# Optimization experiments

Measured on AMD Instinct MI355X. Metric: run time of the kernel, lower is better.

## Reference

```python
import jax, jax.numpy as jnp
import numpy as np

V, E, H, K, B, T = 50000, 128, 256, 9, 128, 512
HD = H // 2  # hidden per direction


def setup_inputs() -> dict:
    key = jax.random.key(0)
    ks = jax.random.split(key, 16)
    s = 0.1
    inp = {
        "x": jax.random.randint(ks[0], (B, T), 0, V),
        "emb": jax.random.normal(ks[1], (V, E), jnp.float32) * 0.02,
        "w_ih_f": jax.random.normal(ks[2], (4 * HD, E), jnp.float32) * s,
        "w_hh_f": jax.random.normal(ks[3], (4 * HD, HD), jnp.float32) * s,
        "b_ih_f": jax.random.normal(ks[4], (4 * HD,), jnp.float32) * s,
        "b_hh_f": jax.random.normal(ks[5], (4 * HD,), jnp.float32) * s,
        "w_ih_b": jax.random.normal(ks[6], (4 * HD, E), jnp.float32) * s,
        "w_hh_b": jax.random.normal(ks[7], (4 * HD, HD), jnp.float32) * s,
        "b_ih_b": jax.random.normal(ks[8], (4 * HD,), jnp.float32) * s,
        "b_hh_b": jax.random.normal(ks[9], (4 * HD,), jnp.float32) * s,
        "W_tag": jax.random.normal(ks[10], (K, H), jnp.float32) * s,
        "b_tag": jax.random.normal(ks[11], (K,), jnp.float32) * s,
        "start_trans": jax.random.normal(ks[12], (K,), jnp.float32) * s,
        "end_trans": jax.random.normal(ks[13], (K,), jnp.float32) * s,
        "trans": jax.random.normal(ks[14], (K, K), jnp.float32) * s,
    }
    return inp


def _lstm_dir(xs, w_ih, w_hh, b_ih, b_hh, reverse):
    # xs: [T, B, E]; PyTorch gate order: i, f, g, o
    Bsz = xs.shape[1]
    hd = w_hh.shape[1]
    b = b_ih + b_hh

    def step(carry, x_t):
        h, c = carry
        gates = x_t @ w_ih.T + h @ w_hh.T + b  # [B, 4*hd]
        i, f, g, o = jnp.split(gates, 4, axis=-1)
        i = jax.nn.sigmoid(i)
        f = jax.nn.sigmoid(f)
        g = jnp.tanh(g)
        o = jax.nn.sigmoid(o)
        c = f * c + i * g
        h = o * jnp.tanh(c)
        return (h, c), h

    init = (jnp.zeros((Bsz, hd), xs.dtype), jnp.zeros((Bsz, hd), xs.dtype))
    _, hs = jax.lax.scan(step, init, xs, reverse=reverse)
    return hs  # [T, B, hd], time-ordered


def _viterbi(emissions, start_trans, end_trans, trans):
    # emissions: [T, B, K]; returns best tag path [B, T] (torchcrf decode, no mask)
    score0 = start_trans[None, :] + emissions[0]  # [B, K]

    def step(score, emis_t):
        # score[b, i] + trans[i, j] -> best over i
        cand = score[:, :, None] + trans[None, :, :]  # [B, K, K]
        bp = jnp.argmax(cand, axis=1)                 # [B, K] best prev tag
        best = jnp.max(cand, axis=1)
        return best + emis_t, bp

    final_score, bps = jax.lax.scan(step, score0, emissions[1:])  # bps: [T-1, B, K]
    final_score = final_score + end_trans[None, :]
    last_tag = jnp.argmax(final_score, axis=-1)  # [B]

    def back(tag, bp):
        prev = jnp.take_along_axis(bp, tag[:, None], axis=1)[:, 0]
        return prev, prev

    _, path = jax.lax.scan(back, last_tag, bps, reverse=True)  # [T-1, B]
    tags = jnp.concatenate([path, last_tag[None, :]], axis=0)  # [T, B]
    return tags.T.astype(jnp.int32)  # [B, T]


def reference(x, emb, w_ih_f, w_hh_f, b_ih_f, b_hh_f,
              w_ih_b, w_hh_b, b_ih_b, b_hh_b,
              W_tag, b_tag, start_trans, end_trans, trans):
    xt = x.T                        # [T, B]
    e = emb[xt]                     # [T, B, E] embedding gather
    h_f = _lstm_dir(e, w_ih_f, w_hh_f, b_ih_f, b_hh_f, reverse=False)
    h_b = _lstm_dir(e, w_ih_b, w_hh_b, b_ih_b, b_hh_b, reverse=True)
    h = jnp.concatenate([h_f, h_b], axis=-1)  # [T, B, H]
    # dropout is identity at inference
    emissions = h @ W_tag.T + b_tag           # [T, B, K]
    return _viterbi(emissions, start_trans, end_trans, trans)
```

## Files before the change

kernel.cpp:

```cpp
#include <hip/hip_runtime.h>
#include <math.h>

#define TT 512
#define BB 128
#define KK 9

__device__ __forceinline__ float fast_sigmoid(float x) {
    const float LOG2E = 1.4426950408889634f;
    float e = __builtin_amdgcn_exp2f(-x * LOG2E);
    return __builtin_amdgcn_rcpf(1.0f + e);
}
__device__ __forceinline__ float fast_tanh(float x) {
    const float LOG2E = 1.4426950408889634f;
    float a = fabsf(x);
    float e = __builtin_amdgcn_exp2f(-2.0f * a * LOG2E);
    float t = (1.0f - e) * __builtin_amdgcn_rcpf(1.0f + e);
    return copysignf(t, x);
}

__global__ __launch_bounds__(256) void gather_e(
    const int* __restrict__ x, const float* __restrict__ emb,
    float* __restrict__ e)
{
    const int row  = blockIdx.x * 8 + (threadIdx.x >> 5);
    const int lane = threadIdx.x & 31;
    const int t = row >> 7;
    const int b = row & 127;
    const int tok = x[b * TT + t];
    const float4 v = *(const float4*)(emb + (size_t)tok * 128 + lane * 4);
    *(float4*)(e + (size_t)row * 128 + lane * 4) = v;
}

__global__ __launch_bounds__(256, 1) void input_gemm(
    const float* __restrict__ e,
    const float* __restrict__ w_ih_f, const float* __restrict__ w_ih_b,
    const float* __restrict__ b_ih_f, const float* __restrict__ b_hh_f,
    const float* __restrict__ b_ih_b, const float* __restrict__ b_hh_b,
    float* __restrict__ buf_f, float* __restrict__ buf_b,
    int t0f, int t0b)
{
    const int dir = blockIdx.z;
    const int s   = blockIdx.x;
    const int n0  = blockIdx.y * 128;
    const int t   = (dir ? t0b : t0f) + s;
    const float* w  = dir ? w_ih_b : w_ih_f;
    const float* bi = dir ? b_ih_b : b_ih_f;
    const float* bh = dir ? b_hh_b : b_hh_f;
    float* dst = dir ? buf_b : buf_f;

    __shared__ __align__(16) float As[128][132];
    __shared__ __align__(16) float Bs[128][4][36];

    const int tid = threadIdx.x;
    const int tx = tid & 15;
    const int ty = tid >> 4;
    const int li = tid & 127;
    const int kb = (tid >> 7) * 4;

    const float* arow = e + ((size_t)t * 128 + li) * 128;
    const float* wrow = w + (size_t)(n0 + li) * 128;

    float4 aR[16], bR[16];
    #pragma unroll
    for (int r = 0; r < 16; r++) aR[r] = *(const float4*)(arow + r * 8 + kb);
    #pragma unroll
    for (int r = 0; r < 16; r++) bR[r] = *(const float4*)(wrow + r * 8 + kb);

    const int bsub = li >> 5, boff = li & 31;
    #pragma unroll
    for (int r = 0; r < 16; r++) {
        As[r * 8 + kb + 0][li] = aR[r].x;
        As[r * 8 + kb + 1][li] = aR[r].y;
        As[r * 8 + kb + 2][li] = aR[r].z;
        As[r * 8 + kb + 3][li] = aR[r].w;
        Bs[r * 8 + kb + 0][bsub][boff] = bR[r].x;
        Bs[r * 8 + kb + 1][bsub][boff] = bR[r].y;
        Bs[r * 8 + kb + 2][bsub][boff] = bR[r].z;
        Bs[r * 8 + kb + 3][bsub][boff] = bR[r].w;
    }
    __syncthreads();

    float acc[8][8];
    #pragma unroll
    for (int i = 0; i < 8; i++)
        #pragma unroll
        for (int j = 0; j < 8; j++) acc[i][j] = 0.0f;

    #pragma unroll 8
    for (int k = 0; k < 128; k++) {
        float4 af0 = *(const float4*)&As[k][ty * 8];
        float4 af1 = *(const float4*)&As[k][ty * 8 + 4];
        float4 bf0 = *(const float4*)&Bs[k][tx >> 2][(tx & 3) * 8];
        float4 bf1 = *(const float4*)&Bs[k][tx >> 2][(tx & 3) * 8 + 4];
        float a_[8] = {af0.x, af0.y, af0.z, af0.w, af1.x, af1.y, af1.z, af1.w};
        float b_[8] = {bf0.x, bf0.y, bf0.z, bf0.w, bf1.x, bf1.y, bf1.z, bf1.w};
        #pragma unroll
        for (int i = 0; i < 8; i++)
            #pragma unroll
            for (int j = 0; j < 8; j++)
                acc[i][j] += a_[i] * b_[j];
    }

    const int nbase = n0 + tx * 8;
    float bias[8];
    #pragma unroll
    for (int j = 0; j < 8; j++) {
        int n = nbase + j;
        bias[j] = bi[n] + bh[n];
    }
    #pragma unroll
    for (int i = 0; i < 8; i++) {
        int brow = ty * 8 + i;
        float* o = dst + ((size_t)s * 128 + brow) * 512 + nbase;
        float4 v0, v1;
        v0.x = acc[i][0] + bias[0]; v0.y = acc[i][1] + bias[1];
        v0.z = acc[i][2] + bias[2]; v0.w = acc[i][3] + bias[3];
        v1.x = acc[i][4] + bias[4]; v1.y = acc[i][5] + bias[5];
        v1.z = acc[i][6] + bias[6]; v1.w = acc[i][7] + bias[7];
        *(float4*)o = v0;
        *(float4*)(o + 4) = v1;
    }
}

__global__ __launch_bounds__(512, 2) void lstm_chunk(
    const float* __restrict__ buf_f, const float* __restrict__ buf_b,
    const float* __restrict__ w_hh_f, const float* __restrict__ w_hh_b,
    float* __restrict__ h_all,
    float* __restrict__ h_state, float* __restrict__ c_state,
    int t0f, int t0b, int C, int init)
{
    const int dir = blockIdx.x >> 7;
    const int b   = blockIdx.x & 127;
    const int j   = threadIdx.x;
    const int w_  = j >> 6;
    const int l   = j & 63;
    const int m   = l >> 2;
    const int q   = l & 3;
    const int k   = w_ * 16 + m;
    const int r   = q * 128 + k;

    const float* whh = dir ? w_hh_b : w_hh_f;
    float wR[128];
    #pragma unroll
    for (int qq = 0; qq < 32; qq++) {
        float4 v = *(const float4*)(whh + (size_t)r * 128 + qq * 4);
        wR[4*qq+0] = v.x; wR[4*qq+1] = v.y; wR[4*qq+2] = v.z; wR[4*qq+3] = v.w;
    }

    __shared__ __align__(16) float h_lds[2][128];
    float c;
    if (init) {
        c = 0.0f;
        if (q == 0) h_lds[0][k] = 0.0f;
    } else {
        c = c_state[((size_t)dir * 128 + b) * 128 + k];
        if (q == 0) h_lds[0][k] = h_state[((size_t)dir * 128 + b) * 128 + k];
    }
    __syncthreads();

    const float* buf = dir ? buf_b : buf_f;
    const int t0     = dir ? t0b : t0f;
    const int  tl0   = dir ? (C - 1) : 0;
    const long lstep = dir ? -(long)(128 * 512) : (long)(128 * 512);

    const float* xp = buf + ((size_t)tl0 * 128 + b) * 512 + r;
    float xw = *xp;
    float h_reg = 0.0f;
    int   t_prev = 0;
    bool  have_store = false;

    for (int s = 0; s < C; s++) {
        const int t = t0 + (dir ? (C - 1 - s) : s);
        const int p = s & 1;
        const float* hprev = h_lds[p];

        float a0 = 0.f, a1 = 0.f, a2 = 0.f, a3 = 0.f;
        #pragma unroll
        for (int qq = 0; qq < 32; qq++) {
            float4 h4 = *(const float4*)&hprev[4 * qq];
            a0 += wR[4*qq+0] * h4.x;
            a1 += wR[4*qq+1] * h4.y;
            a2 += wR[4*qq+2] * h4.z;
            a3 += wR[4*qq+3] * h4.w;
        }
        float pre = xw + ((a0 + a1) + (a2 + a3));

        float act = (q == 2) ? fast_tanh(pre) : fast_sigmoid(pre);

        float f_ = __shfl_xor(act, 1);
        float g_ = __shfl_xor(act, 2);
        float o_ = __shfl_xor(act, 3);

        c = f_ * c + act * g_;
        h_reg = o_ * fast_tanh(c);
        if (q == 0) h_lds[p ^ 1][k] = h_reg;

        __syncthreads();

        if (s + 1 < C) { xp += lstep; xw = *xp; }
        if (q == 0)
            h_all[((size_t)t * BB + b) * 256 + dir * 128 + k] = h_reg;
        t_prev = t; have_store = true;
        (void)t_prev; (void)have_store;
    }

    if (q == 0) {
        h_state[((size_t)dir * 128 + b) * 128 + k] = h_reg;
        c_state[((size_t)dir * 128 + b) * 128 + k] = c;
    }
}

__global__ __launch_bounds__(256) void emis_kernel(
    const float* __restrict__ h_all, const float* __restrict__ W_tag,
    const float* __restrict__ b_tag, float* __restrict__ em_sum)
{
    const int wid  = threadIdx.x >> 6;
    const int lane = threadIdx.x & 63;
    const size_t m = (size_t)blockIdx.x * 4 + wid;
    const float4 hv = *(const float4*)(h_all + m * 256 + lane * 4);
    #pragma unroll
    for (int kk = 0; kk < KK; kk++) {
        const float4 wv = *(const float4*)(W_tag + kk * 256 + lane * 4);
        float p = hv.x * wv.x + hv.y * wv.y + hv.z * wv.z + hv.w * wv.w;
        #pragma unroll
        for (int off = 32; off > 0; off >>= 1) p += __shfl_down(p, off);
        if (lane == 0) em_sum[m * KK + kk] = p + b_tag[kk];
    }
}

__global__ __launch_bounds__(64) void viterbi_kernel(
    const float* __restrict__ em_sum,
    const float* __restrict__ start_trans, const float* __restrict__ end_trans,
    const float* __restrict__ trans, int* __restrict__ out)
{
    const int b = blockIdx.x;
    const int lane = threadIdx.x;
    __shared__ float em_s[TT * KK];
    __shared__ unsigned char bp[TT][KK];

    for (int f = lane; f < TT * KK; f += 64) {
        int t = f / KK, kk = f - t * KK;
        em_s[f] = em_sum[((size_t)t * BB + b) * KK + kk];
    }
    __syncthreads();

    float trans_col[KK];
    float score = -1e30f;
    if (lane < KK) {
        #pragma unroll
        for (int i = 0; i < KK; i++) trans_col[i] = trans[i * KK + lane];
        score = start_trans[lane] + em_s[lane];
    }

    for (int t = 1; t < TT; t++) {
        float my = (lane < KK) ? score : -1e30f;
        float sarr[KK];
        #pragma unroll
        for (int i = 0; i < KK; i++) sarr[i] = __shfl(my, i);
        float best = -1e30f;
        int bi = 0;
        #pragma unroll
        for (int i = 0; i < KK; i++) {
            float cand = sarr[i] + trans_col[i];
            if (cand > best) { best = cand; bi = i; }
        }
        if (lane < KK) {
            bp[t][lane] = (unsigned char)bi;
            score = best + em_s[t * KK + lane];
        }
    }

    float fin = (lane < KK) ? (score + end_trans[lane]) : -1e30f;
    float farr[KK];
    #pragma unroll
    for (int jx = 0; jx < KK; jx++) farr[jx] = __shfl(fin, jx);
    float bestf = -1e30f;
    int bj = 0;
    #pragma unroll
    for (int jx = 0; jx < KK; jx++) {
        if (farr[jx] > bestf) { bestf = farr[jx]; bj = jx; }
    }

    if (lane == 0) {
        int tag = bj;
        out[b * TT + (TT - 1)] = tag;
        for (int t = TT - 1; t >= 1; t--) {
            tag = bp[t][tag];
            out[b * TT + t - 1] = tag;
        }
    }
}

extern "C" void kernel_launch(void* const* d_in, const int* in_sizes, int n_in,
                              void* d_out, int out_size, void* d_ws, size_t ws_size,
                              hipStream_t stream)
{
    const int*   x       = (const int*)  d_in[0];
    const float* emb     = (const float*)d_in[1];
    const float* w_ih_f  = (const float*)d_in[2];
    const float* w_hh_f  = (const float*)d_in[3];
    const float* b_ih_f  = (const float*)d_in[4];
    const float* b_hh_f  = (const float*)d_in[5];
    const float* w_ih_b  = (const float*)d_in[6];
    const float* w_hh_b  = (const float*)d_in[7];
    const float* b_ih_b  = (const float*)d_in[8];
    const float* b_hh_b  = (const float*)d_in[9];
    const float* W_tag   = (const float*)d_in[10];
    const float* b_tag   = (const float*)d_in[11];
    const float* start_t = (const float*)d_in[12];
    const float* end_t   = (const float*)d_in[13];
    const float* trans   = (const float*)d_in[14];
    int* out = (int*)d_out;

    const size_t e_elems     = (size_t)TT * BB * 128;
    const size_t hall_elems  = (size_t)TT * BB * 256;
    const size_t em_elems    = (size_t)TT * BB * KK;
    const size_t state_elems = (size_t)2 * 128 * 128;

    int C = 32;
    const int cands[5] = {512, 256, 128, 64, 32};
    for (int ci = 0; ci < 5; ci++) {
        size_t need = ((size_t)2 * cands[ci] * BB * 512
                       + e_elems + hall_elems + em_elems
                       + 2 * state_elems) * sizeof(float);
        if (ws_size >= need) { C = cands[ci]; break; }
    }

    float* buf_f   = (float*)d_ws;
    float* buf_b   = buf_f + (size_t)C * BB * 512;
    float* em_sum  = buf_b + (size_t)C * BB * 512;
    float* h_state = em_sum + em_elems;
    float* c_state = h_state + state_elems;
    float* e       = c_state + state_elems;
    float* h_all   = e + e_elems;

    gather_e<<<dim3((TT * BB) / 8), dim3(256), 0, stream>>>(x, emb, e);

    const int rounds = TT / C;
    for (int r = 0; r < rounds; r++) {
        const int t0f = r * C;
        const int t0b = TT - (r + 1) * C;
        dim3 gg(C, 4, 2);
        input_gemm<<<gg, dim3(256), 0, stream>>>(
            e, w_ih_f, w_ih_b, b_ih_f, b_hh_f, b_ih_b, b_hh_b,
            buf_f, buf_b, t0f, t0b);
        lstm_chunk<<<dim3(256), dim3(512), 0, stream>>>(
            buf_f, buf_b, w_hh_f, w_hh_b, h_all,
            h_state, c_state, t0f, t0b, C, (r == 0) ? 1 : 0);
    }
    emis_kernel<<<dim3((TT * BB) / 4), dim3(256), 0, stream>>>(
        h_all, W_tag, b_tag, em_sum);
    viterbi_kernel<<<dim3(BB), dim3(64), 0, stream>>>(
        em_sum, start_t, end_t, trans, out);
}
```

Baseline: 1.027 ms.

## Fuse embedding gather into input GEMM with swizzled k-major LDS tiles

Removes the separate gather_e kernel and its intermediate buffer: input_gemm now reads token ids and gathers embedding rows directly into LDS. The LDS tiles switch to row-major with an XOR swizzle and float4 reads along k, so the inner loop does four multiply-adds per loaded pair instead of one. Viterbi's argmax over 9 candidates becomes a tree reduction, shortening the serial dependency chain. In exchange, each direction's GEMM gathers embeddings twice, and the swizzled float4 LDS reads may still cause bank conflicts.

```diff
diff --git a/kernel.cpp b/kernel.cpp
--- a/kernel.cpp
+++ b/kernel.cpp
@@ -18,21 +18,8 @@
     return copysignf(t, x);
 }
 
-__global__ __launch_bounds__(256) void gather_e(
+__global__ __launch_bounds__(256, 1) void input_gemm(
     const int* __restrict__ x, const float* __restrict__ emb,
-    float* __restrict__ e)
-{
-    const int row  = blockIdx.x * 8 + (threadIdx.x >> 5);
-    const int lane = threadIdx.x & 31;
-    const int t = row >> 7;
-    const int b = row & 127;
-    const int tok = x[b * TT + t];
-    const float4 v = *(const float4*)(emb + (size_t)tok * 128 + lane * 4);
-    *(float4*)(e + (size_t)row * 128 + lane * 4) = v;
-}
-
-__global__ __launch_bounds__(256, 1) void input_gemm(
-    const float* __restrict__ e,
     const float* __restrict__ w_ih_f, const float* __restrict__ w_ih_b,
     const float* __restrict__ b_ih_f, const float* __restrict__ b_hh_f,
     const float* __restrict__ b_ih_b, const float* __restrict__ b_hh_b,
@@ -48,37 +35,30 @@
     const float* bh = dir ? b_hh_b : b_hh_f;
     float* dst = dir ? buf_b : buf_f;
 
-    __shared__ __align__(16) float As[128][132];
-    __shared__ __align__(16) float Bs[128][4][36];
-
-    const int tid = threadIdx.x;
+    __shared__ __align__(16) float As[128][136];
+    __shared__ __align__(16) float Bs[128][136];
+    __shared__ int tok_s[128];
+
+    const int tid  = threadIdx.x;
+    const int rsub = tid >> 5;
+    const int koff = (tid & 31) * 4;
+
+    if (tid < 128) tok_s[tid] = x[tid * TT + t];
+    __syncthreads();
+
+    #pragma unroll
+    for (int it = 0; it < 16; it++) {
+        const int row = it * 8 + rsub;
+        const int swz = (it & 7) * 4;
+        const float4 av = *(const float4*)(emb + (size_t)tok_s[row] * 128 + koff);
+        const float4 bv = *(const float4*)(w + (size_t)(n0 + row) * 128 + koff);
+        *(float4*)&As[row][koff ^ swz] = av;
+        *(float4*)&Bs[row][koff ^ swz] = bv;
+    }
+    __syncthreads();
+
     const int tx = tid & 15;
     const int ty = tid >> 4;
-    const int li = tid & 127;
-    const int kb = (tid >> 7) * 4;
-
-    const float* arow = e + ((size_t)t * 128 + li) * 128;
-    const float* wrow = w + (size_t)(n0 + li) * 128;
-
-    float4 aR[16], bR[16];
-    #pragma unroll
-    for (int r = 0; r < 16; r++) aR[r] = *(const float4*)(arow + r * 8 + kb);
-    #pragma unroll
-    for (int r = 0; r < 16; r++) bR[r] = *(const float4*)(wrow + r * 8 + kb);
-
-    const int bsub = li >> 5, boff = li & 31;
-    #pragma unroll
-    for (int r = 0; r < 16; r++) {
-        As[r * 8 + kb + 0][li] = aR[r].x;
-        As[r * 8 + kb + 1][li] = aR[r].y;
-        As[r * 8 + kb + 2][li] = aR[r].z;
-        As[r * 8 + kb + 3][li] = aR[r].w;
-        Bs[r * 8 + kb + 0][bsub][boff] = bR[r].x;
-        Bs[r * 8 + kb + 1][bsub][boff] = bR[r].y;
-        Bs[r * 8 + kb + 2][bsub][boff] = bR[r].z;
-        Bs[r * 8 + kb + 3][bsub][boff] = bR[r].w;
-    }
-    __syncthreads();
 
     float acc[8][8];
     #pragma unroll
@@ -86,19 +66,24 @@
         #pragma unroll
         for (int j = 0; j < 8; j++) acc[i][j] = 0.0f;
 
-    #pragma unroll 8
-    for (int k = 0; k < 128; k++) {
-        float4 af0 = *(const float4*)&As[k][ty * 8];
-        float4 af1 = *(const float4*)&As[k][ty * 8 + 4];
-        float4 bf0 = *(const float4*)&Bs[k][tx >> 2][(tx & 3) * 8];
-        float4 bf1 = *(const float4*)&Bs[k][tx >> 2][(tx & 3) * 8 + 4];
-        float a_[8] = {af0.x, af0.y, af0.z, af0.w, af1.x, af1.y, af1.z, af1.w};
-        float b_[8] = {bf0.x, bf0.y, bf0.z, bf0.w, bf1.x, bf1.y, bf1.z, bf1.w};
+    const int swzA = (ty & 7) * 4;
+    const int swzB = (tx & 7) * 4;
+
+    #pragma unroll 4
+    for (int k4 = 0; k4 < 32; k4++) {
+        const int kA = (k4 * 4) ^ swzA;
+        const int kB = (k4 * 4) ^ swzB;
+        float4 a4[8], b4[8];
+        #pragma unroll
+        for (int i = 0; i < 8; i++) a4[i] = *(const float4*)&As[ty * 8 + i][kA];
+        #pragma unroll
+        for (int j = 0; j < 8; j++) b4[j] = *(const float4*)&Bs[tx * 8 + j][kB];
         #pragma unroll
         for (int i = 0; i < 8; i++)
             #pragma unroll
             for (int j = 0; j < 8; j++)
-                acc[i][j] += a_[i] * b_[j];
+                acc[i][j] += a4[i].x * b4[j].x + a4[i].y * b4[j].y
+                           + a4[i].z * b4[j].z + a4[i].w * b4[j].w;
     }
 
     const int nbase = n0 + tx * 8;
@@ -166,8 +151,6 @@
     const float* xp = buf + ((size_t)tl0 * 128 + b) * 512 + r;
     float xw = *xp;
     float h_reg = 0.0f;
-    int   t_prev = 0;
-    bool  have_store = false;
 
     for (int s = 0; s < C; s++) {
         const int t = t0 + (dir ? (C - 1 - s) : s);
@@ -200,8 +183,6 @@
         if (s + 1 < C) { xp += lstep; xw = *xp; }
         if (q == 0)
             h_all[((size_t)t * BB + b) * 256 + dir * 128 + k] = h_reg;
-        t_prev = t; have_store = true;
-        (void)t_prev; (void)have_store;
     }
 
     if (q == 0) {
@@ -228,6 +209,13 @@
     }
 }
 
+__device__ __forceinline__ void vmax(float va, int ia, float vb, int ib,
+                                     float& vo, int& io) {
+    bool gt = vb > va;
+    vo = gt ? vb : va;
+    io = gt ? ib : ia;
+}
+
 __global__ __launch_bounds__(64) void viterbi_kernel(
     const float* __restrict__ em_sum,
     const float* __restrict__ start_trans, const float* __restrict__ end_trans,
@@ -254,19 +242,24 @@
 
     for (int t = 1; t < TT; t++) {
         float my = (lane < KK) ? score : -1e30f;
-        float sarr[KK];
-        #pragma unroll
-        for (int i = 0; i < KK; i++) sarr[i] = __shfl(my, i);
-        float best = -1e30f;
-        int bi = 0;
-        #pragma unroll
-        for (int i = 0; i < KK; i++) {
-            float cand = sarr[i] + trans_col[i];
-            if (cand > best) { best = cand; bi = i; }
-        }
+        float cand[KK];
+        #pragma unroll
+        for (int i = 0; i < KK; i++) cand[i] = __shfl(my, i) + trans_col[i];
+
+        float v01, v23, v45, v67, v03, v47, v07, vb_;
+        int   i01, i23, i45, i67, i03, i47, i07, ib_;
+        vmax(cand[0], 0, cand[1], 1, v01, i01);
+        vmax(cand[2], 2, cand[3], 3, v23, i23);
+        vmax(cand[4], 4, cand[5], 5, v45, i45);
+        vmax(cand[6], 6, cand[7], 7, v67, i67);
+        vmax(v01, i01, v23, i23, v03, i03);
+        vmax(v45, i45, v67, i67, v47, i47);
+        vmax(v03, i03, v47, i47, v07, i07);
+        vmax(v07, i07, cand[8], 8, vb_, ib_);
+
         if (lane < KK) {
-            bp[t][lane] = (unsigned char)bi;
-            score = best + em_s[t * KK + lane];
+            bp[t][lane] = (unsigned char)ib_;
+            score = vb_ + em_s[t * KK + lane];
         }
     }
 
@@ -274,12 +267,16 @@
     float farr[KK];
     #pragma unroll
     for (int jx = 0; jx < KK; jx++) farr[jx] = __shfl(fin, jx);
-    float bestf = -1e30f;
-    int bj = 0;
-    #pragma unroll
-    for (int jx = 0; jx < KK; jx++) {
-        if (farr[jx] > bestf) { bestf = farr[jx]; bj = jx; }
-    }
+    float v01, v23, v45, v67, v03, v47, v07, vb_;
+    int   i01, i23, i45, i67, i03, i47, i07, bj;
+    vmax(farr[0], 0, farr[1], 1, v01, i01);
+    vmax(farr[2], 2, farr[3], 3, v23, i23);
+    vmax(farr[4], 4, farr[5], 5, v45, i45);
+    vmax(farr[6], 6, farr[7], 7, v67, i67);
+    vmax(v01, i01, v23, i23, v03, i03);
+    vmax(v45, i45, v67, i67, v47, i47);
+    vmax(v03, i03, v47, i47, v07, i07);
+    vmax(v07, i07, farr[8], 8, vb_, bj);
 
     if (lane == 0) {
         int tag = bj;
@@ -312,7 +309,6 @@
     const float* trans   = (const float*)d_in[14];
     int* out = (int*)d_out;
 
-    const size_t e_elems     = (size_t)TT * BB * 128;
     const size_t hall_elems  = (size_t)TT * BB * 256;
     const size_t em_elems    = (size_t)TT * BB * KK;
     const size_t state_elems = (size_t)2 * 128 * 128;
@@ -321,7 +317,7 @@
     const int cands[5] = {512, 256, 128, 64, 32};
     for (int ci = 0; ci < 5; ci++) {
         size_t need = ((size_t)2 * cands[ci] * BB * 512
-                       + e_elems + hall_elems + em_elems
+                       + hall_elems + em_elems
                        + 2 * state_elems) * sizeof(float);
         if (ws_size >= need) { C = cands[ci]; break; }
     }
@@ -331,10 +327,7 @@
     float* em_sum  = buf_b + (size_t)C * BB * 512;
     float* h_state = em_sum + em_elems;
     float* c_state = h_state + state_elems;
-    float* e       = c_state + state_elems;
-    float* h_all   = e + e_elems;
-
-    gather_e<<<dim3((TT * BB) / 8), dim3(256), 0, stream>>>(x, emb, e);
+    float* h_all   = c_state + state_elems;
 
     const int rounds = TT / C;
     for (int r = 0; r < rounds; r++) {
@@ -342,7 +335,7 @@
         const int t0b = TT - (r + 1) * C;
         dim3 gg(C, 4, 2);
         input_gemm<<<gg, dim3(256), 0, stream>>>(
-            e, w_ih_f, w_ih_b, b_ih_f, b_hh_f, b_ih_b, b_hh_b,
+            x, emb, w_ih_f, w_ih_b, b_ih_f, b_hh_f, b_ih_b, b_hh_b,
             buf_f, buf_b, t0f, t0b);
         lstm_chunk<<<dim3(256), dim3(512), 0, stream>>>(
             buf_f, buf_b, w_hh_f, w_hh_b, h_all,
```

Result: slower. 1.056 ms (+2.9%).
